# Optimization experiments

Measured on AMD Instinct MI355X. Metric: run time of the kernel, lower is better.

Reference implementation:

```python
import jax, jax.numpy as jnp
import numpy as np


def _pool_axis(x, out_size, axis):
    # AdaptiveMaxPool along one axis, PyTorch bin semantics:
    # bin i = [floor(i*H/o), ceil((i+1)*H/o))
    x = jnp.moveaxis(x, axis, 0)
    H = x.shape[0]
    o = np.arange(out_size)
    starts = (o * H) // out_size
    ends = -((-(o + 1) * H) // out_size)
    L = int((ends - starts).max())
    idx = np.minimum(starts[:, None] + np.arange(L)[None, :], H - 1)  # (o, L)
    mask = np.arange(L)[None, :] < (ends - starts)[:, None]
    xg = x[jnp.asarray(idx)]  # (o, L, ...)
    neg = jnp.finfo(x.dtype).min
    m = jnp.asarray(mask).reshape(mask.shape + (1,) * (xg.ndim - 2))
    out = jnp.where(m, xg, neg).max(axis=1)  # (o, ...)
    return jnp.moveaxis(out, 0, axis)


def adaptive_max_pool2d(x, oh, ow):  # x: (C, H, W)
    return _pool_axis(_pool_axis(x, oh, 1), ow, 2)


def graph_conv(h, src, dst, W, b, N):
    # DGL GraphConv, norm='both': D_out^{-1/2} A D_in^{-1/2} h W + b
    ones = jnp.ones(src.shape, h.dtype)
    out_deg = jax.ops.segment_sum(ones, src, num_segments=N)
    in_deg = jax.ops.segment_sum(ones, dst, num_segments=N)
    ns = jax.lax.rsqrt(jnp.maximum(out_deg, 1.0))
    nd = jax.lax.rsqrt(jnp.maximum(in_deg, 1.0))
    hp = (h * ns[:, None]) @ W  # project first (in_dim >= out_dim)
    agg = jax.ops.segment_sum(hp[src], dst, num_segments=N)
    return agg * nd[:, None] + b


def setup_inputs() -> dict:
    key = jax.random.key(0)
    ks = jax.random.split(key, 16)
    N, E, in_dim, hd, B, n_classes = 50000, 1600000, 128, 32, 256, 2
    p = lambda k, shp: (jax.random.normal(k, shp, jnp.float32) * 0.05)
    return {
        'x': jax.random.normal(ks[0], (N, in_dim), jnp.float32),
        'src': jax.random.randint(ks[1], (E,), 0, N, jnp.int32),
        'dst': jax.random.randint(ks[2], (E,), 0, N, jnp.int32),
        'num_graphs': B,
        'W1': p(ks[3], (in_dim, hd)), 'b1': p(ks[4], (hd,)),
        'W2': p(ks[5], (hd, hd)), 'b2': p(ks[6], (hd,)),
        'W3': p(ks[7], (hd, hd)), 'b3': p(ks[8], (hd,)),
        'W4': p(ks[9], (hd, hd)), 'b4': p(ks[10], (hd,)),
        'Wamp': p(ks[11], (hd * hd, hd)), 'bamp': p(ks[12], (hd,)),
        'Wc': p(ks[13], (hd, n_classes)), 'bc': p(ks[14], (n_classes,)),
    }


def reference(x, src, dst, num_graphs, W1, b1, W2, b2, W3, b3, W4, b4, Wamp, bamp, Wc, bc):
    N = x.shape[0]
    h1 = jax.nn.relu(graph_conv(x, src, dst, W1, b1, N))
    h2 = jax.nn.relu(graph_conv(h1, src, dst, W2, b2, N))
    h3 = jax.nn.relu(graph_conv(h2, src, dst, W3, b3, N))
    h4 = jax.nn.relu(graph_conv(h3, src, dst, W4, b4, N))  # dropout is eval-mode identity
    h_concat = jnp.concatenate([h1, h2, h3, h4], axis=1)  # (N, 128)
    hc = h_concat.reshape(32, N, 4)
    aux = adaptive_max_pool2d(hc, num_graphs, 32)  # (32, B, 32)
    h_features = aux.reshape(num_graphs, -1)  # (B, 1024)
    h = jax.nn.relu(h_features @ Wamp + bamp)  # conv1Damp, kernel=1 -> matmul
    classification = h @ Wc + bc
    return classification, h_concat, h_features
```

## Files before the change

kernel.cpp:

```cpp
#include <hip/hip_runtime.h>
#include <hip/hip_bf16.h>
#include <hip/hip_fp16.h>
#include <float.h>

#define BGRAPHS 256
#define NCHUNK 32
#define NSLICE 8
#define NSMAX  6272

__device__ __forceinline__ int chunk_bound(int c, int nchunks, int E) {
    if (c >= nchunks) return E;
    return (int)(((long long)c * E / nchunks) & ~3LL);
}

__global__ __launch_bounds__(1024) void k_hist(const int* __restrict__ src,
                                               const int* __restrict__ dst,
                                               unsigned* __restrict__ partials,
                                               int E, int N) {
    __shared__ unsigned hist[NSMAX];
    int g = blockIdx.x % NSLICE;
    int c = blockIdx.x / NSLICE;
    int nchunks = gridDim.x / NSLICE;
    int NS = (N + NSLICE - 1) / NSLICE;
    int lo = g * NS;
    int hi = min(N, lo + NS);
    int tid = threadIdx.x;
    for (int i = tid; i < NS; i += 1024) hist[i] = 0u;
    __syncthreads();
    int e0 = chunk_bound(c, nchunks, E);
    int e1 = chunk_bound(c + 1, nchunks, E);
    int nvec = (e1 - e0) & ~3;
    for (int e = e0 + tid * 4; e < e0 + nvec; e += 4096) {
        int4 s4 = *(const int4*)(src + e);
        int4 d4 = *(const int4*)(dst + e);
        if (s4.x >= lo && s4.x < hi) atomicAdd(&hist[s4.x - lo], 1u << 16);
        if (s4.y >= lo && s4.y < hi) atomicAdd(&hist[s4.y - lo], 1u << 16);
        if (s4.z >= lo && s4.z < hi) atomicAdd(&hist[s4.z - lo], 1u << 16);
        if (s4.w >= lo && s4.w < hi) atomicAdd(&hist[s4.w - lo], 1u << 16);
        if (d4.x >= lo && d4.x < hi) atomicAdd(&hist[d4.x - lo], 1u);
        if (d4.y >= lo && d4.y < hi) atomicAdd(&hist[d4.y - lo], 1u);
        if (d4.z >= lo && d4.z < hi) atomicAdd(&hist[d4.z - lo], 1u);
        if (d4.w >= lo && d4.w < hi) atomicAdd(&hist[d4.w - lo], 1u);
    }
    for (int e = e0 + nvec + tid; e < e1; e += 1024) {
        int s = src[e], d = dst[e];
        if (s >= lo && s < hi) atomicAdd(&hist[s - lo], 1u << 16);
        if (d >= lo && d < hi) atomicAdd(&hist[d - lo], 1u);
    }
    __syncthreads();
    for (int i = tid; i < hi - lo; i += 1024)
        partials[(size_t)c * N + lo + i] = hist[i];
}

__global__ void k_scan(unsigned* __restrict__ partials,
                       int* __restrict__ start, int* __restrict__ ind,
                       int* __restrict__ counter,
                       float* __restrict__ ns, float* __restrict__ nd, int N) {
    int n = blockIdx.x * 256 + threadIdx.x;
    int lane = threadIdx.x & 63;
    unsigned run = 0, so = 0;
    if (n < N) {
        #pragma unroll 8
        for (int c = 0; c < NCHUNK; c++) {
            unsigned v = partials[(size_t)c * N + n];
            partials[(size_t)c * N + n] = run;
            run += v & 0xFFFFu;
            so  += v >> 16;
        }
        ind[n] = (int)run;
        ns[n] = rsqrtf(fmaxf((float)so, 1.f));
        nd[n] = rsqrtf(fmaxf((float)run, 1.f));
    }
    int d = (n < N) ? (int)run : 0;
    int s = d;
    #pragma unroll
    for (int off = 1; off < 64; off <<= 1) {
        int t = __shfl_up(s, off);
        if (lane >= off) s += t;
    }
    int total = __shfl(s, 63);
    int base = 0;
    if (lane == 63) base = atomicAdd(counter, total);
    base = __shfl(base, 63);
    if (n < N) start[n] = base + s - d;
}

__global__ __launch_bounds__(1024) void k_fill2(const int* __restrict__ src,
                                                const int* __restrict__ dst,
                                                const int* __restrict__ start,
                                                const unsigned* __restrict__ partials,
                                                int* __restrict__ csr, int E, int N) {
    __shared__ int base[NSMAX];
    int g = blockIdx.x % NSLICE;
    int c = blockIdx.x / NSLICE;
    int nchunks = gridDim.x / NSLICE;
    int NS = (N + NSLICE - 1) / NSLICE;
    int lo = g * NS;
    int hi = min(N, lo + NS);
    int tid = threadIdx.x;
    for (int i = tid; i < hi - lo; i += 1024)
        base[i] = start[lo + i] + (int)partials[(size_t)c * N + lo + i];
    __syncthreads();
    int e0 = chunk_bound(c, nchunks, E);
    int e1 = chunk_bound(c + 1, nchunks, E);
    int nvec = (e1 - e0) & ~3;
    for (int e = e0 + tid * 4; e < e0 + nvec; e += 4096) {
        int4 d4 = *(const int4*)(dst + e);
        int4 s4 = *(const int4*)(src + e);
        if (d4.x >= lo && d4.x < hi) csr[atomicAdd(&base[d4.x - lo], 1)] = s4.x;
        if (d4.y >= lo && d4.y < hi) csr[atomicAdd(&base[d4.y - lo], 1)] = s4.y;
        if (d4.z >= lo && d4.z < hi) csr[atomicAdd(&base[d4.z - lo], 1)] = s4.z;
        if (d4.w >= lo && d4.w < hi) csr[atomicAdd(&base[d4.w - lo], 1)] = s4.w;
    }
    for (int e = e0 + nvec + tid; e < e1; e += 1024) {
        int d = dst[e];
        if (d >= lo && d < hi) csr[atomicAdd(&base[d - lo], 1)] = src[e];
    }
}

__global__ __launch_bounds__(256) void k_proj1(const float* __restrict__ x,
                                               const float* __restrict__ ns,
                                               const float* __restrict__ W,
                                               __half* __restrict__ hp, int N) {
    __shared__ float sW[128 * 32];
    __shared__ float sx[8 * 128];
    int tid = threadIdx.x;
    const float4* W4 = (const float4*)W;
    float4* sW4 = (float4*)sW;
    #pragma unroll
    for (int i = tid; i < 1024; i += 256) sW4[i] = W4[i];
    int base = blockIdx.x * 8;
    {
        int r = tid >> 5;
        int node = base + r;
        if (node < N) ((float4*)sx)[tid] = ((const float4*)x)[node * 32 + (tid & 31)];
    }
    __syncthreads();
    int r = tid >> 5, j = tid & 31;
    int node = base + r;
    if (node >= N) return;
    float s = ns[node];
    float acc = 0.f;
    #pragma unroll 8
    for (int k = 0; k < 128; k++) acc += sx[r * 128 + k] * sW[k * 32 + j];
    hp[node * 32 + j] = __float2half(acc * s);
}

template <bool PROJ>
__global__ __launch_bounds__(256) void k_gf(const __half* __restrict__ hp,
                                            const int* __restrict__ csr,
                                            const int* __restrict__ start,
                                            const int* __restrict__ degi,
                                            const float* __restrict__ ndv,
                                            const float* __restrict__ nsv,
                                            const float* __restrict__ b,
                                            const float* __restrict__ W,
                                            float* __restrict__ hcat, int loff,
                                            __half* __restrict__ hp_next,
                                            int N, int nWaves) {
    int lane = threadIdx.x & 63;
    int f = lane & 31, pair = lane >> 5;
    float wreg[16];
    if (PROJ) {
        #pragma unroll
        for (int kk = 0; kk < 16; kk++) wreg[kk] = W[(pair * 16 + kk) * 32 + f];
    }
    float bias = b[f];
    int wid = blockIdx.x * 4 + (threadIdx.x >> 6);
    for (int n = wid; n < N; n += nWaves) {
        int s0 = start[n];
        int deg = degi[n];
        int i = s0 + pair, end = s0 + deg;
        float acc = 0.f;
        for (; i + 6 < end; i += 8) {
            int a0 = csr[i], a1 = csr[i + 2], a2 = csr[i + 4], a3 = csr[i + 6];
            float v0 = __half2float(hp[a0 * 32 + f]);
            float v1 = __half2float(hp[a1 * 32 + f]);
            float v2 = __half2float(hp[a2 * 32 + f]);
            float v3 = __half2float(hp[a3 * 32 + f]);
            acc += v0 + v1 + v2 + v3;
        }
        for (; i < end; i += 2) acc += __half2float(hp[csr[i] * 32 + f]);
        acc += __shfl_xor(acc, 32);
        float h = fmaxf(acc * ndv[n] + bias, 0.f);
        if (lane < 32) hcat[(size_t)n * 128 + loff + f] = h;
        if (PROJ) {
            float acc2 = 0.f;
            #pragma unroll
            for (int kk = 0; kk < 16; kk++)
                acc2 += __shfl(h, pair * 16 + kk) * wreg[kk];
            acc2 += __shfl_xor(acc2, 32);
            if (lane < 32) hp_next[n * 32 + f] = __float2half(acc2 * nsv[n]);
        }
    }
}

__global__ __launch_bounds__(256) void k_pool(const float* __restrict__ hcat,
                                              float* __restrict__ hfeat, int N) {
    int p = blockIdx.x * 4 + (threadIdx.x >> 6);
    int lane = threadIdx.x & 63;
    int a = p >> 8, bb = p & 255;
    int s = (bb * N) >> 8;
    int e = ((bb + 1) * N + 255) >> 8;
    const float4* base4 = ((const float4*)hcat) + (size_t)a * N;
    float4 mx = make_float4(-FLT_MAX, -FLT_MAX, -FLT_MAX, -FLT_MAX);
    for (int m = s + lane; m < e; m += 64) {
        float4 v = base4[m];
        mx.x = fmaxf(mx.x, v.x);
        mx.y = fmaxf(mx.y, v.y);
        mx.z = fmaxf(mx.z, v.z);
        mx.w = fmaxf(mx.w, v.w);
    }
    #pragma unroll
    for (int off = 32; off; off >>= 1) {
        mx.x = fmaxf(mx.x, __shfl_xor(mx.x, off));
        mx.y = fmaxf(mx.y, __shfl_xor(mx.y, off));
        mx.z = fmaxf(mx.z, __shfl_xor(mx.z, off));
        mx.w = fmaxf(mx.w, __shfl_xor(mx.w, off));
    }
    if (lane < 32) {
        int g = (a << 3) + (bb >> 5);
        int f0 = (bb & 31) << 5;
        float v = (lane < 8) ? mx.x : (lane < 16) ? mx.y : (lane < 24) ? mx.z : mx.w;
        hfeat[g * 1024 + f0 + lane] = v;
    }
}

__global__ __launch_bounds__(256) void k_amp(const float* __restrict__ hf,
                                             const float* __restrict__ Wamp,
                                             const float* __restrict__ bamp,
                                             const float* __restrict__ Wc,
                                             const float* __restrict__ bc,
                                             float* __restrict__ out) {
    __shared__ float part[256];
    __shared__ float sham[32];
    int g = blockIdx.x;
    int tid = threadIdx.x;
    int j = tid & 31, c = tid >> 5;
    const float* hrow = hf + g * 1024;
    float acc = 0.f;
    int k0 = c * 128;
    #pragma unroll 4
    for (int k = k0; k < k0 + 128; k++) acc += hrow[k] * Wamp[k * 32 + j];
    part[tid] = acc;
    __syncthreads();
    if (tid < 32) {
        float s = part[tid];
        #pragma unroll
        for (int c2 = 1; c2 < 8; c2++) s += part[tid + (c2 << 5)];
        sham[tid] = fmaxf(s + bamp[tid], 0.f);
    }
    __syncthreads();
    if (tid < 2) {
        float a2 = bc[tid];
        #pragma unroll
        for (int k = 0; k < 32; k++) a2 += sham[k] * Wc[k * 2 + tid];
        out[g * 2 + tid] = a2;
    }
}

extern "C" void kernel_launch(void* const* d_in, const int* in_sizes, int n_in,
                              void* d_out, int out_size, void* d_ws, size_t ws_size,
                              hipStream_t stream) {
    const float* x    = (const float*)d_in[0];
    const int*   src  = (const int*)d_in[1];
    const int*   dst  = (const int*)d_in[2];
    const float* W1   = (const float*)d_in[4];
    const float* b1   = (const float*)d_in[5];
    const float* W2   = (const float*)d_in[6];
    const float* b2   = (const float*)d_in[7];
    const float* W3   = (const float*)d_in[8];
    const float* b3   = (const float*)d_in[9];
    const float* W4   = (const float*)d_in[10];
    const float* b4   = (const float*)d_in[11];
    const float* Wamp = (const float*)d_in[12];
    const float* bamp = (const float*)d_in[13];
    const float* Wc   = (const float*)d_in[14];
    const float* bc   = (const float*)d_in[15];

    const int N = in_sizes[0] / 128;
    const int E = in_sizes[1];

    float* out   = (float*)d_out;
    float* cls   = out;
    float* hcat  = out + 512;
    float* hfeat = out + 512 + (size_t)N * 128;

    char* w = (char*)d_ws;
    int*    counter = (int*)w;    w += 64;
    int*    start   = (int*)w;    w += (size_t)N * 4;
    int*    ind_i   = (int*)w;    w += (size_t)N * 4;
    float*  ns      = (float*)w;  w += (size_t)N * 4;
    float*  ndv     = (float*)w;  w += (size_t)N * 4;
    int*    csr     = (int*)w;    w += (size_t)E * 4;
    __half* hpA     = (__half*)w; w += (size_t)N * 32 * 2;
    __half* hpB     = (__half*)w; w += (size_t)N * 32 * 2;
    unsigned* partials = (unsigned*)hpA;

    hipMemsetAsync(counter, 0, 64, stream);

    const int GB_BUILD = NCHUNK * NSLICE;
    k_hist <<<GB_BUILD, 1024, 0, stream>>>(src, dst, partials, E, N);
    k_scan <<<(N + 255) / 256, 256, 0, stream>>>(partials, start, ind_i, counter, ns, ndv, N);
    k_fill2<<<GB_BUILD, 1024, 0, stream>>>(src, dst, start, partials, csr, E, N);

    k_proj1<<<(N + 7) / 8, 256, 0, stream>>>(x, ns, W1, hpA, N);

    const int GB = 2048, NW = GB * 4;
    k_gf<true ><<<GB, 256, 0, stream>>>(hpA, csr, start, ind_i, ndv, ns, b1, W2, hcat, 0,  hpB, N, NW);
    k_gf<true ><<<GB, 256, 0, stream>>>(hpB, csr, start, ind_i, ndv, ns, b2, W3, hcat, 32, hpA, N, NW);
    k_gf<true ><<<GB, 256, 0, stream>>>(hpA, csr, start, ind_i, ndv, ns, b3, W4, hcat, 64, hpB, N, NW);
    k_gf<false><<<GB, 256, 0, stream>>>(hpB, csr, start, ind_i, ndv, ns, b4, nullptr, hcat, 96, nullptr, N, NW);

    k_pool<<<(32 * BGRAPHS) / 4, 256, 0, stream>>>(hcat, hfeat, N);

    k_amp<<<BGRAPHS, 256, 0, stream>>>(hfeat, Wamp, bamp, Wc, bc, cls);
}
```

Baseline: 334.9 us.

## Vectorize gather in k_gf, fuse pool+amp head, drop memset, double chunks

The graph aggregation kernel now has each lane load 8 bytes (four half features) per edge and spreads 8 edges across the wave, where before each lane loaded one half per edge, cutting the number of gather instructions. The projection to the next layer is rebuilt around float4 weights and a shuffle reduction. The pooling and MLP head kernels are merged into one per-graph kernel that keeps pooled features in shared memory. The counter memset becomes a write inside k_hist, and NCHUNK doubles with partials moved to their own workspace region. The merged head launches only 256 blocks, and the counter reset relies on k_hist finishing before k_scan reads it.

```diff
diff --git a/kernel.cpp b/kernel.cpp
--- a/kernel.cpp
+++ b/kernel.cpp
@@ -4,7 +4,7 @@
 #include <float.h>
 
 #define BGRAPHS 256
-#define NCHUNK 32
+#define NCHUNK 64
 #define NSLICE 8
 #define NSMAX  6272
 
@@ -16,6 +16,7 @@
 __global__ __launch_bounds__(1024) void k_hist(const int* __restrict__ src,
                                                const int* __restrict__ dst,
                                                unsigned* __restrict__ partials,
+                                               int* __restrict__ counter,
                                                int E, int N) {
     __shared__ unsigned hist[NSMAX];
     int g = blockIdx.x % NSLICE;
@@ -25,6 +26,7 @@
     int lo = g * NS;
     int hi = min(N, lo + NS);
     int tid = threadIdx.x;
+    if (blockIdx.x == 0 && tid == 0) counter[0] = 0;
     for (int i = tid; i < NS; i += 1024) hist[i] = 0u;
     __syncthreads();
     int e0 = chunk_bound(c, nchunks, E);
@@ -158,104 +160,144 @@
                                             float* __restrict__ hcat, int loff,
                                             __half* __restrict__ hp_next,
                                             int N, int nWaves) {
+    const float2* hp4 = (const float2*)hp;
     int lane = threadIdx.x & 63;
-    int f = lane & 31, pair = lane >> 5;
-    float wreg[16];
+    int t = lane & 7, g = lane >> 3;
+    float4 wreg[4];
     if (PROJ) {
         #pragma unroll
-        for (int kk = 0; kk < 16; kk++) wreg[kk] = W[(pair * 16 + kk) * 32 + f];
-    }
-    float bias = b[f];
+        for (int j = 0; j < 4; j++)
+            wreg[j] = *(const float4*)&W[(4 * g + j) * 32 + 4 * t];
+    }
+    float4 bias = *(const float4*)&b[4 * t];
     int wid = blockIdx.x * 4 + (threadIdx.x >> 6);
     for (int n = wid; n < N; n += nWaves) {
         int s0 = start[n];
-        int deg = degi[n];
-        int i = s0 + pair, end = s0 + deg;
-        float acc = 0.f;
-        for (; i + 6 < end; i += 8) {
-            int a0 = csr[i], a1 = csr[i + 2], a2 = csr[i + 4], a3 = csr[i + 6];
-            float v0 = __half2float(hp[a0 * 32 + f]);
-            float v1 = __half2float(hp[a1 * 32 + f]);
-            float v2 = __half2float(hp[a2 * 32 + f]);
-            float v3 = __half2float(hp[a3 * 32 + f]);
-            acc += v0 + v1 + v2 + v3;
-        }
-        for (; i < end; i += 2) acc += __half2float(hp[csr[i] * 32 + f]);
-        acc += __shfl_xor(acc, 32);
-        float h = fmaxf(acc * ndv[n] + bias, 0.f);
-        if (lane < 32) hcat[(size_t)n * 128 + loff + f] = h;
+        int end = s0 + degi[n];
+        float4 acc = make_float4(0.f, 0.f, 0.f, 0.f);
+        int i = s0 + g;
+        for (; i + 8 < end; i += 16) {
+            int a0 = csr[i], a1 = csr[i + 8];
+            float2 r0 = hp4[a0 * 8 + t];
+            float2 r1 = hp4[a1 * 8 + t];
+            float2 p00 = __half22float2(*(__half2*)&r0.x);
+            float2 p01 = __half22float2(*(__half2*)&r0.y);
+            float2 p10 = __half22float2(*(__half2*)&r1.x);
+            float2 p11 = __half22float2(*(__half2*)&r1.y);
+            acc.x += p00.x + p10.x; acc.y += p00.y + p10.y;
+            acc.z += p01.x + p11.x; acc.w += p01.y + p11.y;
+        }
+        for (; i < end; i += 8) {
+            float2 r = hp4[csr[i] * 8 + t];
+            float2 p0 = __half22float2(*(__half2*)&r.x);
+            float2 p1 = __half22float2(*(__half2*)&r.y);
+            acc.x += p0.x; acc.y += p0.y; acc.z += p1.x; acc.w += p1.y;
+        }
+        #pragma unroll
+        for (int off = 8; off <= 32; off <<= 1) {
+            acc.x += __shfl_xor(acc.x, off);
+            acc.y += __shfl_xor(acc.y, off);
+            acc.z += __shfl_xor(acc.z, off);
+            acc.w += __shfl_xor(acc.w, off);
+        }
+        float ndn = ndv[n];
+        float4 h;
+        h.x = fmaxf(acc.x * ndn + bias.x, 0.f);
+        h.y = fmaxf(acc.y * ndn + bias.y, 0.f);
+        h.z = fmaxf(acc.z * ndn + bias.z, 0.f);
+        h.w = fmaxf(acc.w * ndn + bias.w, 0.f);
+        if (lane < 8)
+            *(float4*)(hcat + (size_t)n * 128 + loff + 4 * t) = h;
         if (PROJ) {
-            float acc2 = 0.f;
+            float4 p = make_float4(0.f, 0.f, 0.f, 0.f);
+            {
+                float hk0 = __shfl(h.x, g), hk1 = __shfl(h.y, g);
+                float hk2 = __shfl(h.z, g), hk3 = __shfl(h.w, g);
+                p.x = hk0 * wreg[0].x + hk1 * wreg[1].x + hk2 * wreg[2].x + hk3 * wreg[3].x;
+                p.y = hk0 * wreg[0].y + hk1 * wreg[1].y + hk2 * wreg[2].y + hk3 * wreg[3].y;
+                p.z = hk0 * wreg[0].z + hk1 * wreg[1].z + hk2 * wreg[2].z + hk3 * wreg[3].z;
+                p.w = hk0 * wreg[0].w + hk1 * wreg[1].w + hk2 * wreg[2].w + hk3 * wreg[3].w;
+            }
             #pragma unroll
-            for (int kk = 0; kk < 16; kk++)
-                acc2 += __shfl(h, pair * 16 + kk) * wreg[kk];
-            acc2 += __shfl_xor(acc2, 32);
-            if (lane < 32) hp_next[n * 32 + f] = __float2half(acc2 * nsv[n]);
-        }
-    }
-}
-
-__global__ __launch_bounds__(256) void k_pool(const float* __restrict__ hcat,
-                                              float* __restrict__ hfeat, int N) {
-    int p = blockIdx.x * 4 + (threadIdx.x >> 6);
-    int lane = threadIdx.x & 63;
-    int a = p >> 8, bb = p & 255;
-    int s = (bb * N) >> 8;
-    int e = ((bb + 1) * N + 255) >> 8;
-    const float4* base4 = ((const float4*)hcat) + (size_t)a * N;
-    float4 mx = make_float4(-FLT_MAX, -FLT_MAX, -FLT_MAX, -FLT_MAX);
-    for (int m = s + lane; m < e; m += 64) {
-        float4 v = base4[m];
-        mx.x = fmaxf(mx.x, v.x);
-        mx.y = fmaxf(mx.y, v.y);
-        mx.z = fmaxf(mx.z, v.z);
-        mx.w = fmaxf(mx.w, v.w);
-    }
-    #pragma unroll
-    for (int off = 32; off; off >>= 1) {
-        mx.x = fmaxf(mx.x, __shfl_xor(mx.x, off));
-        mx.y = fmaxf(mx.y, __shfl_xor(mx.y, off));
-        mx.z = fmaxf(mx.z, __shfl_xor(mx.z, off));
-        mx.w = fmaxf(mx.w, __shfl_xor(mx.w, off));
-    }
-    if (lane < 32) {
-        int g = (a << 3) + (bb >> 5);
-        int f0 = (bb & 31) << 5;
-        float v = (lane < 8) ? mx.x : (lane < 16) ? mx.y : (lane < 24) ? mx.z : mx.w;
-        hfeat[g * 1024 + f0 + lane] = v;
-    }
-}
-
-__global__ __launch_bounds__(256) void k_amp(const float* __restrict__ hf,
-                                             const float* __restrict__ Wamp,
-                                             const float* __restrict__ bamp,
-                                             const float* __restrict__ Wc,
-                                             const float* __restrict__ bc,
-                                             float* __restrict__ out) {
+            for (int off = 8; off <= 32; off <<= 1) {
+                p.x += __shfl_xor(p.x, off);
+                p.y += __shfl_xor(p.y, off);
+                p.z += __shfl_xor(p.z, off);
+                p.w += __shfl_xor(p.w, off);
+            }
+            if (lane < 8) {
+                float nsn = nsv[n];
+                float2 st;
+                *(__half2*)&st.x = __floats2half2_rn(p.x * nsn, p.y * nsn);
+                *(__half2*)&st.y = __floats2half2_rn(p.z * nsn, p.w * nsn);
+                ((float2*)hp_next)[n * 8 + t] = st;
+            }
+        }
+    }
+}
+
+__global__ __launch_bounds__(256) void k_head(const float* __restrict__ hcat,
+                                              const float* __restrict__ Wamp,
+                                              const float* __restrict__ bamp,
+                                              const float* __restrict__ Wc,
+                                              const float* __restrict__ bc,
+                                              float* __restrict__ hfeat,
+                                              float* __restrict__ out, int N) {
+    __shared__ float shf[1024];
     __shared__ float part[256];
     __shared__ float sham[32];
-    int g = blockIdx.x;
+    int gph = blockIdx.x;
+    int a = gph >> 3;
     int tid = threadIdx.x;
-    int j = tid & 31, c = tid >> 5;
-    const float* hrow = hf + g * 1024;
+    int lane = tid & 63, w = tid >> 6;
+    const float4* base4 = ((const float4*)hcat) + (size_t)a * N;
+    #pragma unroll
+    for (int q = 0; q < 8; q++) {
+        int j = w * 8 + q;
+        int bb = ((gph & 7) << 5) + j;
+        int s = (bb * N) >> 8;
+        int e = ((bb + 1) * N + 255) >> 8;
+        float4 mx = make_float4(-FLT_MAX, -FLT_MAX, -FLT_MAX, -FLT_MAX);
+        for (int m = s + lane; m < e; m += 64) {
+            float4 v = base4[m];
+            mx.x = fmaxf(mx.x, v.x);
+            mx.y = fmaxf(mx.y, v.y);
+            mx.z = fmaxf(mx.z, v.z);
+            mx.w = fmaxf(mx.w, v.w);
+        }
+        #pragma unroll
+        for (int off = 32; off; off >>= 1) {
+            mx.x = fmaxf(mx.x, __shfl_xor(mx.x, off));
+            mx.y = fmaxf(mx.y, __shfl_xor(mx.y, off));
+            mx.z = fmaxf(mx.z, __shfl_xor(mx.z, off));
+            mx.w = fmaxf(mx.w, __shfl_xor(mx.w, off));
+        }
+        if (lane < 32) {
+            float v = (lane < 8) ? mx.x : (lane < 16) ? mx.y : (lane < 24) ? mx.z : mx.w;
+            shf[j * 32 + lane] = v;
+            hfeat[gph * 1024 + j * 32 + lane] = v;
+        }
+    }
+    __syncthreads();
+    int jj = tid & 31, c = tid >> 5;
     float acc = 0.f;
     int k0 = c * 128;
     #pragma unroll 4
-    for (int k = k0; k < k0 + 128; k++) acc += hrow[k] * Wamp[k * 32 + j];
+    for (int k = k0; k < k0 + 128; k++) acc += shf[k] * Wamp[k * 32 + jj];
     part[tid] = acc;
     __syncthreads();
     if (tid < 32) {
-        float s = part[tid];
-        #pragma unroll
-        for (int c2 = 1; c2 < 8; c2++) s += part[tid + (c2 << 5)];
-        sham[tid] = fmaxf(s + bamp[tid], 0.f);
+        float s2 = part[tid];
+        #pragma unroll
+        for (int c2 = 1; c2 < 8; c2++) s2 += part[tid + (c2 << 5)];
+        sham[tid] = fmaxf(s2 + bamp[tid], 0.f);
     }
     __syncthreads();
     if (tid < 2) {
         float a2 = bc[tid];
         #pragma unroll
         for (int k = 0; k < 32; k++) a2 += sham[k] * Wc[k * 2 + tid];
-        out[g * 2 + tid] = a2;
+        out[gph * 2 + tid] = a2;
     }
 }
 
@@ -287,20 +329,18 @@
     float* hfeat = out + 512 + (size_t)N * 128;
 
     char* w = (char*)d_ws;
-    int*    counter = (int*)w;    w += 64;
-    int*    start   = (int*)w;    w += (size_t)N * 4;
-    int*    ind_i   = (int*)w;    w += (size_t)N * 4;
-    float*  ns      = (float*)w;  w += (size_t)N * 4;
-    float*  ndv     = (float*)w;  w += (size_t)N * 4;
-    int*    csr     = (int*)w;    w += (size_t)E * 4;
-    __half* hpA     = (__half*)w; w += (size_t)N * 32 * 2;
-    __half* hpB     = (__half*)w; w += (size_t)N * 32 * 2;
-    unsigned* partials = (unsigned*)hpA;
-
-    hipMemsetAsync(counter, 0, 64, stream);
+    int*      counter  = (int*)w;      w += 64;
+    int*      start    = (int*)w;      w += (size_t)N * 4;
+    int*      ind_i    = (int*)w;      w += (size_t)N * 4;
+    float*    ns       = (float*)w;    w += (size_t)N * 4;
+    float*    ndv      = (float*)w;    w += (size_t)N * 4;
+    int*      csr      = (int*)w;      w += (size_t)E * 4;
+    __half*   hpA      = (__half*)w;   w += (size_t)N * 32 * 2;
+    __half*   hpB      = (__half*)w;   w += (size_t)N * 32 * 2;
+    unsigned* partials = (unsigned*)w; w += (size_t)NCHUNK * N * 4;
 
     const int GB_BUILD = NCHUNK * NSLICE;
-    k_hist <<<GB_BUILD, 1024, 0, stream>>>(src, dst, partials, E, N);
+    k_hist <<<GB_BUILD, 1024, 0, stream>>>(src, dst, partials, counter, E, N);
     k_scan <<<(N + 255) / 256, 256, 0, stream>>>(partials, start, ind_i, counter, ns, ndv, N);
     k_fill2<<<GB_BUILD, 1024, 0, stream>>>(src, dst, start, partials, csr, E, N);
 
@@ -312,7 +352,5 @@
     k_gf<true ><<<GB, 256, 0, stream>>>(hpA, csr, start, ind_i, ndv, ns, b3, W4, hcat, 64, hpB, N, NW);
     k_gf<false><<<GB, 256, 0, stream>>>(hpB, csr, start, ind_i, ndv, ns, b4, nullptr, hcat, 96, nullptr, N, NW);
 
-    k_pool<<<(32 * BGRAPHS) / 4, 256, 0, stream>>>(hcat, hfeat, N);
-
-    k_amp<<<BGRAPHS, 256, 0, stream>>>(hfeat, Wamp, bamp, Wc, bc, cls);
-}
+    k_head<<<BGRAPHS, 256, 0, stream>>>(hcat, Wamp, bamp, Wc, bc, hfeat, cls, N);
+}
```

Measured after the change: 307.1 us. 8.3% less time.
